# Performance work log

Measured on AMD Instinct MI355X. Metric: run time of the kernel, lower is better.

Reference implementation:

```python
import jax, jax.numpy as jnp
import numpy as np

B, C, W, H = 4, 256, 64, 64
N = W * H
SCALE = 0.02  # keep QK^T energies in a stable softmax range


def setup_inputs() -> dict:
    key = jax.random.key(0)
    ks = jax.random.split(key, 8)
    return {
        "x": jax.random.normal(ks[0], (B, C, W, H), jnp.float32),
        "geo_embed": jax.random.normal(ks[1], (B, N, C), jnp.float32),
        "Wq": jax.random.normal(ks[2], (C, C), jnp.float32) * SCALE,
        "bq": jnp.zeros((C,), jnp.float32),
        "Wk": jax.random.normal(ks[3], (C, C), jnp.float32) * SCALE,
        "bk": jnp.zeros((C,), jnp.float32),
        "Wv": jax.random.normal(ks[4], (C, C), jnp.float32) * SCALE,
        "bv": jnp.zeros((C,), jnp.float32),
        "Wgp": jax.random.normal(ks[5], (C, C), jnp.float32) * SCALE,
        "bgp": jnp.zeros((C,), jnp.float32),
        "Wgg": jax.random.normal(ks[6], (1, 2 * C), jnp.float32) * SCALE,
        "bgg": jnp.zeros((1,), jnp.float32),
    }


def reference(x, geo_embed, Wq, bq, Wk, bk, Wv, bv, Wgp, bgp, Wgg, bgg):
    b, c, w, h = x.shape
    n = w * h
    xf = x.reshape(b, c, n)  # [B, C, N]

    # 1x1 conv == per-pixel linear; q laid out [B, N, O] (permuted in torch)
    q = jnp.einsum("oc,bcn->bno", Wq, xf) + bq  # [B, N, O]

    # geo gating on the query
    ge = geo_embed @ Wgp.T + bgp  # [B, N, O]
    gate = jax.nn.sigmoid(jnp.concatenate([q, ge], axis=-1) @ Wgg.T + bgg)  # [B, N, 1]
    q = q + gate * ge

    k = jnp.einsum("oc,bcn->bon", Wk, xf) + bk[:, None]  # [B, O, N]
    v = jnp.einsum("oc,bcn->bon", Wv, xf) + bv[:, None]  # [B, C, N]

    energy = jnp.einsum("bno,bom->bnm", q, k)  # [B, N, N]
    attention = jax.nn.softmax(energy, axis=-1)

    # out = bmm(value, attention^T): out[b,c,m] = sum_n v[b,c,n] * attention[b,m,n]
    out = jnp.einsum("bcn,bmn->bcm", v, attention).reshape(b, c, w, h)

    # output gating: torch .view reinterpretation of (B, N, O) as (B, C, W, H)
    ge_r = ge.reshape(b, c, w, h)
    out = out * (1.0 + jax.nn.sigmoid(ge_r))
    return out, attention
```

## Files before the change

### kernel.cpp

```cpp
#include <hip/hip_runtime.h>
#include <hip/hip_bf16.h>
#include <math.h>

static constexpr int BB = 4;
static constexpr int CC = 256;
static constexpr int NN = 4096;

using bf16   = __bf16;
using f16    = _Float16;
using bf16x8 = __attribute__((ext_vector_type(8))) __bf16;
using bf16x4 = __attribute__((ext_vector_type(4))) __bf16;
using f16x8  = __attribute__((ext_vector_type(8))) _Float16;
using f16x4  = __attribute__((ext_vector_type(4))) _Float16;
using f32x4  = __attribute__((ext_vector_type(4))) float;

__device__ inline void gload_lds16(const void* g, void* l) {
  __builtin_amdgcn_global_load_lds(
      (const __attribute__((address_space(1))) void*)g,
      (__attribute__((address_space(3))) void*)l, 16, 0, 0);
}

__device__ inline void swz_bid(int& xb, int& yb, int& zb) {
  int gx = gridDim.x, gy = gridDim.y;
  int nwg = gx * gy * (int)gridDim.z;
  int flat = blockIdx.x + gx * (blockIdx.y + gy * blockIdx.z);
  int q = nwg >> 3;
  int w = (flat & 7) * q + (flat >> 3);
  xb = w % gx;
  int r = w / gx;
  yb = r % gy;
  zb = r / gy;
}

__global__ __launch_bounds__(256) void cvt_weights_kernel(
    const float* __restrict__ w0, const float* __restrict__ w1,
    const float* __restrict__ w2, const float* __restrict__ w3,
    bf16* __restrict__ out) {
  const float* srcs[4] = {w0, w1, w2, w3};
  const float* s = srcs[blockIdx.y];
  bf16* dst = out + (size_t)blockIdx.y * (CC * CC);
  int i = (blockIdx.x * 256 + threadIdx.x) * 4;
  float4 v = *(const float4*)(s + i);
  bf16x4 t;
  t[0] = (bf16)v.x; t[1] = (bf16)v.y; t[2] = (bf16)v.z; t[3] = (bf16)v.w;
  *(bf16x4*)(dst + i) = t;
}

__global__ __launch_bounds__(256) void cvt_f32_bf16_kernel(
    const float* __restrict__ in, bf16* __restrict__ out, long n) {
  long i = ((long)blockIdx.x * blockDim.x + threadIdx.x) * 4;
  if (i >= n) return;
  float4 v = *(const float4*)(in + i);
  bf16x4 t;
  t[0] = (bf16)v.x; t[1] = (bf16)v.y; t[2] = (bf16)v.z; t[3] = (bf16)v.w;
  *(bf16x4*)(out + i) = t;
}

__global__ __launch_bounds__(256) void transpose_x_kernel(
    const float* __restrict__ x, bf16* __restrict__ xt) {
  __shared__ float tile[64][65];
  int b  = blockIdx.z;
  int c0 = blockIdx.x * 64;
  int n0 = blockIdx.y * 64;
  const float* xp = x  + (long)b * CC * NN;
  bf16*       xtp = xt + (long)b * NN * CC;
  int tj = threadIdx.x & 63;
  int ti = threadIdx.x >> 6;
#pragma unroll
  for (int p = 0; p < 16; ++p) {
    int i = ti + p * 4;
    tile[i][tj] = xp[(long)(c0 + i) * NN + n0 + tj];
  }
  __syncthreads();
#pragma unroll
  for (int p = 0; p < 16; ++p) {
    int i = ti + p * 4;
    xtp[(long)(n0 + i) * CC + c0 + tj] = (bf16)tile[tj][i];
  }
}

__global__ __launch_bounds__(256) void proj_all_kernel(
    const bf16* __restrict__ xt, const bf16* __restrict__ geob,
    const bf16* __restrict__ Wall,
    const float* __restrict__ bq, const float* __restrict__ bgp,
    const float* __restrict__ bk, const float* __restrict__ bv,
    bf16* __restrict__ qn, float* __restrict__ ge,
    bf16* __restrict__ kn, bf16* __restrict__ vb) {
  __shared__ bf16 As[128 * 32];
  __shared__ bf16 Bs[128 * 32];
  const long NCst = (long)NN * CC;
  const int bz = blockIdx.z;
  const int b = bz >> 2, p = bz & 3;
  const bf16 *Ap, *Bp;
  const float* bias;
  int row0, col0;
  if (p == 3) {
    Ap = Wall + 2 * CC * CC;
    Bp = xt + b * NCst;
    bias = bv;
    row0 = blockIdx.x * 128;
    col0 = blockIdx.y * 128;
  } else {
    Ap = (p == 1 ? geob : xt) + b * NCst;
    Bp = Wall + (size_t)(p == 0 ? 0 : (p == 1 ? 3 : 1)) * CC * CC;
    bias = (p == 0 ? bq : (p == 1 ? bgp : bk));
    row0 = blockIdx.y * 128;
    col0 = blockIdx.x * 128;
  }

  const int t   = threadIdx.x;
  const int wid = t >> 6;
  const int l   = t & 63;
  const int lr  = l & 15;
  const int lk  = (l >> 4) * 8;
  const int warow = (wid >> 1) * 64;
  const int wbcol = (wid & 1) * 64;
  const int srow = t >> 2;
  const int scol = (t & 3) * 8;

  f32x4 acc[4][4];
#pragma unroll
  for (int i = 0; i < 4; ++i)
#pragma unroll
    for (int j = 0; j < 4; ++j) acc[i][j] = {0.f, 0.f, 0.f, 0.f};

  for (int k0 = 0; k0 < CC; k0 += 32) {
    __syncthreads();
#pragma unroll
    for (int q = 0; q < 2; ++q)
      gload_lds16(Ap + (long)(row0 + srow + 64 * q) * CC + k0 + scol,
                  As + ((q * 256 + t) * 8));
#pragma unroll
    for (int q = 0; q < 2; ++q)
      gload_lds16(Bp + (long)(col0 + srow + 64 * q) * CC + k0 + scol,
                  Bs + ((q * 256 + t) * 8));
    __syncthreads();
    bf16x8 a[4], bb[4];
#pragma unroll
    for (int i = 0; i < 4; ++i)
      a[i] = *(const bf16x8*)(As + (warow + 16 * i + lr) * 32 + lk);
#pragma unroll
    for (int j = 0; j < 4; ++j)
      bb[j] = *(const bf16x8*)(Bs + (wbcol + 16 * j + lr) * 32 + lk);
#pragma unroll
    for (int i = 0; i < 4; ++i)
#pragma unroll
      for (int j = 0; j < 4; ++j)
        acc[i][j] = __builtin_amdgcn_mfma_f32_16x16x32_bf16(a[i], bb[j], acc[i][j], 0, 0, 0);
  }

  const int orow = (l >> 4) * 4;
  const int ocol = l & 15;
#pragma unroll
  for (int i = 0; i < 4; ++i) {
#pragma unroll
    for (int j = 0; j < 4; ++j) {
      int colb = col0 + wbcol + 16 * j + ocol;
#pragma unroll
      for (int r = 0; r < 4; ++r) {
        int row = row0 + warow + 16 * i + orow + r;
        if (p == 3) {
          float vv = acc[i][j][r] + bias[row];
          vb[b * NCst + (long)row * NN + colb] = (bf16)vv;
        } else {
          float vv = acc[i][j][r] + bias[colb];
          long di = b * NCst + (long)row * CC + colb;
          if (p == 1)
            ge[di] = vv;
          else
            (p == 0 ? qn : kn)[di] = (bf16)vv;
        }
      }
    }
  }
}

template <int BIAS_MODE, int B_MODE, int OUT_MODE, bool GATE_EPI, bool SWZ, bool STAT>
__global__ __launch_bounds__(256) void gemm_nt_lds(
    const bf16* __restrict__ A, const void* __restrict__ Bm,
    const float* __restrict__ bias, void* __restrict__ D,
    const float* __restrict__ gefl, float2* __restrict__ pstat,
    int Ncols, int K, long sA, long sB, long sD, long sGe) {
  __shared__ bf16 As[128 * 32];
  __shared__ bf16 Bs[128 * 32];
  int bx = blockIdx.x, by = blockIdx.y, bz = blockIdx.z;
  if constexpr (SWZ) swz_bid(bx, by, bz);
  const bf16* Ab = A + (long)bz * sA;
  const float* geb = GATE_EPI ? (gefl + bz * sGe) : nullptr;

  const int t   = threadIdx.x;
  const int wid = t >> 6;
  const int l   = t & 63;
  const int lr  = l & 15;
  const int lk  = (l >> 4) * 8;
  const int row0 = by * 128;
  const int col0 = bx * 128;
  const int warow = (wid >> 1) * 64;
  const int wbcol = (wid & 1) * 64;

  const int srow = t >> 2;
  const int scol = (t & 3) * 8;
  const int frow = t >> 3;
  const int fc4  = (t & 7) * 4;

  f32x4 acc[4][4];
#pragma unroll
  for (int i = 0; i < 4; ++i)
#pragma unroll
    for (int j = 0; j < 4; ++j) acc[i][j] = {0.f, 0.f, 0.f, 0.f};

  for (int k0 = 0; k0 < K; k0 += 32) {
    __syncthreads();
#pragma unroll
    for (int p = 0; p < 2; ++p)
      gload_lds16(Ab + (long)(row0 + srow + 64 * p) * K + k0 + scol,
                  As + ((p * 256 + t) * 8));
    if constexpr (B_MODE == 0) {
      const bf16* Bb = (const bf16*)Bm + (long)bz * sB;
#pragma unroll
      for (int p = 0; p < 2; ++p)
        gload_lds16(Bb + (long)(col0 + srow + 64 * p) * K + k0 + scol,
                    Bs + ((p * 256 + t) * 8));
    } else {
      const float* Bf = (const float*)Bm + (long)bz * sB;
#pragma unroll
      for (int p = 0; p < 4; ++p) {
        float4 u = *(const float4*)(Bf + (long)(col0 + frow + 32 * p) * K + k0 + fc4);
        bf16x4 tv;
        tv[0] = (bf16)u.x; tv[1] = (bf16)u.y; tv[2] = (bf16)u.z; tv[3] = (bf16)u.w;
        *(bf16x4*)(Bs + (frow + 32 * p) * 32 + fc4) = tv;
      }
    }
    __syncthreads();
    bf16x8 a[4], bb[4];
#pragma unroll
    for (int i = 0; i < 4; ++i)
      a[i] = *(const bf16x8*)(As + (warow + 16 * i + lr) * 32 + lk);
#pragma unroll
    for (int j = 0; j < 4; ++j)
      bb[j] = *(const bf16x8*)(Bs + (wbcol + 16 * j + lr) * 32 + lk);
#pragma unroll
    for (int i = 0; i < 4; ++i)
#pragma unroll
      for (int j = 0; j < 4; ++j)
        acc[i][j] = __builtin_amdgcn_mfma_f32_16x16x32_bf16(a[i], bb[j], acc[i][j], 0, 0, 0);
  }

  const int orow = (l >> 4) * 4;
  const int ocol = l & 15;
#pragma unroll
  for (int i = 0; i < 4; ++i) {
#pragma unroll
    for (int j = 0; j < 4; ++j) {
      int colb = col0 + wbcol + 16 * j + ocol;
#pragma unroll
      for (int r = 0; r < 4; ++r) {
        int row = row0 + warow + 16 * i + orow + r;
        float vv = acc[i][j][r];
        if constexpr (BIAS_MODE == 1) vv += bias[colb];
        if constexpr (BIAS_MODE == 2) vv += bias[row];
        if constexpr (GATE_EPI) {
          float g = geb[(long)row * 4096 + colb];
          vv *= 1.f + 1.f / (1.f + __expf(-g));
        }
        long di = bz * sD + (long)row * Ncols + colb;
        if constexpr (OUT_MODE == 0)
          ((float*)D)[di] = vv;
        else if constexpr (OUT_MODE == 1)
          ((bf16*)D)[di] = (bf16)vv;
        else
          ((f16*)D)[di] = (f16)vv;
      }
    }
  }

  if constexpr (STAT) {
    __shared__ float2 sm[128][2];
#pragma unroll
    for (int i = 0; i < 4; ++i) {
#pragma unroll
      for (int r = 0; r < 4; ++r) {
        float m = fmaxf(fmaxf(acc[i][0][r], acc[i][1][r]),
                        fmaxf(acc[i][2][r], acc[i][3][r]));
#pragma unroll
        for (int s = 8; s >= 1; s >>= 1) m = fmaxf(m, __shfl_xor(m, s, 64));
        float sum = 0.f;
#pragma unroll
        for (int j = 0; j < 4; ++j) sum += __expf(acc[i][j][r] - m);
#pragma unroll
        for (int s = 8; s >= 1; s >>= 1) sum += __shfl_xor(sum, s, 64);
        if ((l & 15) == 0) {
          int Rl = warow + 16 * i + (l >> 4) * 4 + r;
          sm[Rl][wid & 1] = make_float2(m, sum);
        }
      }
    }
    __syncthreads();
    if (t < 128) {
      float2 a2 = sm[t][0], b2 = sm[t][1];
      float m = fmaxf(a2.x, b2.x);
      float s = a2.y * __expf(a2.x - m) + b2.y * __expf(b2.x - m);
      pstat[((long)bz * NN + row0 + t) * 32 + bx] = make_float2(m, s);
    }
  }
}

__global__ __launch_bounds__(256) void rowstat_reduce_kernel(
    const float2* __restrict__ pstat, float2* __restrict__ minv) {
  int row = blockIdx.x * 4 + (threadIdx.x >> 6);
  int l = threadIdx.x & 63;
  float2 v = (l < 32) ? pstat[(long)row * 32 + l] : make_float2(-1e30f, 0.f);
  float m = v.x;
#pragma unroll
  for (int s = 16; s >= 1; s >>= 1) m = fmaxf(m, __shfl_xor(m, s, 64));
  float sum = v.y * __expf(v.x - m);
#pragma unroll
  for (int s = 16; s >= 1; s >>= 1) sum += __shfl_xor(sum, s, 64);
  if (l == 0) minv[row] = make_float2(m, 1.f / sum);
}

template <bool SWZ>
__global__ __launch_bounds__(512) void pv_fused_kernel(
    const bf16* __restrict__ V, const f16* __restrict__ E,
    const float2* __restrict__ minv, float* __restrict__ attn,
    float* __restrict__ pbuf) {
  __shared__ bf16 Bs[2][64 * 64];
  int bx = blockIdx.x, by = blockIdx.y, bz = blockIdx.z;
  if constexpr (SWZ) swz_bid(bx, by, bz);
  const int mrow0 = bx * 64;
  const int KBASE = by * (NN / 2);
  const long NCst = (long)NN * CC;
  const long NNst = (long)NN * NN;
  const bf16* Vb = V + bz * NCst;
  const f16*  Eb = E + bz * NNst;
  float* attnb = attn + bz * NNst;
  float* pb = pbuf + (long)(bz * 2 + by) * NCst;

  const int t   = threadIdx.x;
  const int wid = t >> 6;
  const int l   = t & 63;
  const int lr  = l & 15;
  const int lk8 = l >> 4;
  const int crow = wid * 32;

  const int rE = t >> 3;
  const int q4 = (t & 7) * 4;
  const float2 mi = minv[(long)bz * NN + mrow0 + rE];
  const f16* Erow = Eb + (long)(mrow0 + rE) * NN + q4;
  float* Arow = attnb + (long)(mrow0 + rE) * NN + q4;
  const int c8a = (t & 7) >> 1;
  const int o4  = (t & 1) * 4;
  const int woff1 = rE * 64 + ((c8a ^ (rE & 7)) << 3) + o4;
  const int woff2 = rE * 64 + (((c8a + 4) ^ (rE & 7)) << 3) + o4;

  const bf16* Vr0 = Vb + (long)(crow + lr) * NN + lk8 * 8;
  const bf16* Vr1 = Vb + (long)(crow + 16 + lr) * NN + lk8 * 8;

  f32x4 acc[2][4];
#pragma unroll
  for (int i = 0; i < 2; ++i)
#pragma unroll
    for (int j = 0; j < 4; ++j) acc[i][j] = {0.f, 0.f, 0.f, 0.f};

  f16x4 elo = *(const f16x4*)(Erow + KBASE);
  f16x4 ehi = *(const f16x4*)(Erow + KBASE + 32);

  auto produce = [&](int kdst, int buf) {
    float pl[4], ph[4];
#pragma unroll
    for (int i = 0; i < 4; ++i) pl[i] = __expf((float)elo[i] - mi.x) * mi.y;
#pragma unroll
    for (int i = 0; i < 4; ++i) ph[i] = __expf((float)ehi[i] - mi.x) * mi.y;
    float4 u0 = {pl[0], pl[1], pl[2], pl[3]};
    float4 u1 = {ph[0], ph[1], ph[2], ph[3]};
    *(float4*)(Arow + kdst)      = u0;
    *(float4*)(Arow + kdst + 32) = u1;
    bf16x4 b0, b1;
#pragma unroll
    for (int i = 0; i < 4; ++i) { b0[i] = (bf16)pl[i]; b1[i] = (bf16)ph[i]; }
    *(bf16x4*)(&Bs[buf][woff1]) = b0;
    *(bf16x4*)(&Bs[buf][woff2]) = b1;
    int kn = (kdst + 64) & (NN - 1);
    elo = *(const f16x4*)(Erow + kn);
    ehi = *(const f16x4*)(Erow + kn + 32);
  };

  auto consume = [&](int buf, bf16x8 a00, bf16x8 a01, bf16x8 a10, bf16x8 a11) {
    const bf16* B0 = &Bs[buf][0];
#pragma unroll
    for (int j = 0; j < 4; ++j) {
      int Rb = 16 * j + lr;
      bf16x8 b0 = *(const bf16x8*)(B0 + Rb * 64 + ((lk8 ^ (Rb & 7)) * 8));
      bf16x8 b1 = *(const bf16x8*)(B0 + Rb * 64 + (((lk8 + 4) ^ (Rb & 7)) * 8));
      acc[0][j] = __builtin_amdgcn_mfma_f32_16x16x32_bf16(a00, b0, acc[0][j], 0, 0, 0);
      acc[1][j] = __builtin_amdgcn_mfma_f32_16x16x32_bf16(a10, b0, acc[1][j], 0, 0, 0);
      acc[0][j] = __builtin_amdgcn_mfma_f32_16x16x32_bf16(a01, b1, acc[0][j], 0, 0, 0);
      acc[1][j] = __builtin_amdgcn_mfma_f32_16x16x32_bf16(a11, b1, acc[1][j], 0, 0, 0);
    }
  };

#define LOADV(k0, A0, A1, A2, A3)                  \
  A0 = *(const bf16x8*)(Vr0 + (k0));               \
  A1 = *(const bf16x8*)(Vr0 + (k0) + 32);          \
  A2 = *(const bf16x8*)(Vr1 + (k0));               \
  A3 = *(const bf16x8*)(Vr1 + (k0) + 32);

#define FENCE_BAR()                                         \
  asm volatile("s_waitcnt lgkmcnt(0)" ::: "memory");        \
  __builtin_amdgcn_s_barrier();                             \
  __builtin_amdgcn_sched_barrier(0);

  bf16x8 A00, A01, A10, A11, B00, B01, B10, B11;

  produce(KBASE, 0);
  LOADV(KBASE, A00, A01, A10, A11);
  FENCE_BAR();

  for (int it = 0; it < 15; ++it) {
    int k0 = KBASE + it * 128;
    LOADV(k0 + 64, B00, B01, B10, B11);
    consume(0, A00, A01, A10, A11);
    produce(k0 + 64, 1);
    FENCE_BAR();
    LOADV(k0 + 128, A00, A01, A10, A11);
    consume(1, B00, B01, B10, B11);
    produce(k0 + 128, 0);
    FENCE_BAR();
  }
  LOADV(KBASE + 1984, B00, B01, B10, B11);
  consume(0, A00, A01, A10, A11);
  produce(KBASE + 1984, 1);
  FENCE_BAR();
  consume(1, B00, B01, B10, B11);
#undef LOADV
#undef FENCE_BAR

  const int orow = (l >> 4) * 4;
  const int ocol = l & 15;
#pragma unroll
  for (int i = 0; i < 2; ++i) {
#pragma unroll
    for (int j = 0; j < 4; ++j) {
      int m = mrow0 + 16 * j + ocol;
#pragma unroll
      for (int r = 0; r < 4; ++r) {
        int c = crow + 16 * i + orow + r;
        pb[(long)c * 4096 + m] = acc[i][j][r];
      }
    }
  }
}

__global__ __launch_bounds__(256) void combine_kernel(
    const float* __restrict__ pbuf, const float* __restrict__ ge,
    float* __restrict__ out) {
  const long NCst = (long)NN * CC;
  long i = ((long)blockIdx.x * 256 + threadIdx.x) * 8;
  int b = (int)(i >> 20);
  long r = i & (NCst - 1);
  const float* p0 = pbuf + (long)(b * 2) * NCst + r;
  const float* p1 = p0 + NCst;
  const float* g  = ge + (long)b * NCst + r;
  float* o = out + i;
#pragma unroll
  for (int h = 0; h < 2; ++h) {
    float4 a = *(const float4*)(p0 + h * 4);
    float4 c = *(const float4*)(p1 + h * 4);
    float4 gv = *(const float4*)(g + h * 4);
    float4 u;
    u.x = (a.x + c.x) * (1.f + 1.f / (1.f + __expf(-gv.x)));
    u.y = (a.y + c.y) * (1.f + 1.f / (1.f + __expf(-gv.y)));
    u.z = (a.z + c.z) * (1.f + 1.f / (1.f + __expf(-gv.z)));
    u.w = (a.w + c.w) * (1.f + 1.f / (1.f + __expf(-gv.w)));
    *(float4*)(o + h * 4) = u;
  }
}

__global__ __launch_bounds__(256) void gate_kernel(
    bf16* __restrict__ q, const float* __restrict__ ge,
    const float* __restrict__ Wgg, const float* __restrict__ bgg) {
  int row = blockIdx.x * 4 + (threadIdx.x >> 6);
  int l = threadIdx.x & 63;
  bf16* qr = q + (long)row * 256;
  const float* ger = ge + (long)row * 256;
  float s = 0.f;
  float qv[4], gv[4];
#pragma unroll
  for (int i = 0; i < 4; ++i) {
    int o = l + 64 * i;
    qv[i] = (float)qr[o];
    gv[i] = ger[o];
    s += qv[i] * Wgg[o] + gv[i] * Wgg[256 + o];
  }
#pragma unroll
  for (int m = 32; m >= 1; m >>= 1) s += __shfl_xor(s, m, 64);
  float gate = 1.f / (1.f + __expf(-(s + bgg[0])));
#pragma unroll
  for (int i = 0; i < 4; ++i) {
    int o = l + 64 * i;
    qr[o] = (bf16)(qv[i] + gate * gv[i]);
  }
}

__global__ __launch_bounds__(256) void softmax32_kernel(float* __restrict__ attn) {
  long row = blockIdx.x;
  float* p = attn + row * 4096;
  int t = threadIdx.x;
  __shared__ float red[8];
  float4 v[4];
  float mx = -1e30f;
#pragma unroll
  for (int c = 0; c < 4; ++c) {
    v[c] = *(const float4*)(p + c * 1024 + t * 4);
    mx = fmaxf(mx, fmaxf(fmaxf(v[c].x, v[c].y), fmaxf(v[c].z, v[c].w)));
  }
#pragma unroll
  for (int m = 32; m >= 1; m >>= 1) mx = fmaxf(mx, __shfl_xor(mx, m, 64));
  if ((t & 63) == 0) red[t >> 6] = mx;
  __syncthreads();
  mx = fmaxf(fmaxf(red[0], red[1]), fmaxf(red[2], red[3]));
  float sum = 0.f;
#pragma unroll
  for (int c = 0; c < 4; ++c) {
    v[c].x = __expf(v[c].x - mx);
    v[c].y = __expf(v[c].y - mx);
    v[c].z = __expf(v[c].z - mx);
    v[c].w = __expf(v[c].w - mx);
    sum += v[c].x + v[c].y + v[c].z + v[c].w;
  }
#pragma unroll
  for (int m = 32; m >= 1; m >>= 1) sum += __shfl_xor(sum, m, 64);
  if ((t & 63) == 0) red[4 + (t >> 6)] = sum;
  __syncthreads();
  float inv = 1.f / (red[4] + red[5] + red[6] + red[7]);
#pragma unroll
  for (int c = 0; c < 4; ++c) {
    v[c].x *= inv; v[c].y *= inv; v[c].z *= inv; v[c].w *= inv;
    *(float4*)(p + c * 1024 + t * 4) = v[c];
  }
}

extern "C" void kernel_launch(void* const* d_in, const int* in_sizes, int n_in,
                              void* d_out, int out_size, void* d_ws, size_t ws_size,
                              hipStream_t stream) {
  const float* x    = (const float*)d_in[0];
  const float* geo  = (const float*)d_in[1];
  const float* Wq   = (const float*)d_in[2];
  const float* bq   = (const float*)d_in[3];
  const float* Wk   = (const float*)d_in[4];
  const float* bk   = (const float*)d_in[5];
  const float* Wv   = (const float*)d_in[6];
  const float* bv   = (const float*)d_in[7];
  const float* Wgp  = (const float*)d_in[8];
  const float* bgp  = (const float*)d_in[9];
  const float* Wgg  = (const float*)d_in[10];
  const float* bgg  = (const float*)d_in[11];

  float* out  = (float*)d_out;
  float* attn = out + (long)BB * CC * NN;

  char* w = (char*)d_ws;
  size_t used = 0;
  auto alloc = [&](size_t bytes) {
    char* p = w + used;
    used += (bytes + 255) & ~(size_t)255;
    return p;
  };
  bf16*  xt   = (bf16*)alloc((size_t)BB * NN * CC * 2);
  bf16*  geob = (bf16*)alloc((size_t)BB * NN * CC * 2);
  bf16*  qn   = (bf16*)alloc((size_t)BB * NN * CC * 2);
  bf16*  kn   = (bf16*)alloc((size_t)BB * NN * CC * 2);
  bf16*  vb   = (bf16*)alloc((size_t)BB * CC * NN * 2);
  float* ge   = (float*)alloc((size_t)BB * NN * CC * 4);
  bf16*  Wall = (bf16*)alloc((size_t)4 * CC * CC * 2);
  bf16*  Wvb  = Wall + 2 * CC * CC;
  size_t abf_bytes   = (size_t)BB * NN * NN * 2;
  size_t pstat_bytes = (size_t)BB * NN * 32 * sizeof(float2);
  size_t minv_bytes  = (size_t)BB * NN * sizeof(float2);
  size_t pbuf_bytes  = (size_t)BB * 2 * NN * CC * 4;
  bool big = (ws_size >=
              used + abf_bytes + pstat_bytes + minv_bytes + pbuf_bytes + 2048);
  f16* abf = nullptr;
  float2* pstat = nullptr;
  float2* minv = nullptr;
  float* pbuf = nullptr;
  if (big) {
    abf   = (f16*)alloc(abf_bytes);
    pstat = (float2*)alloc(pstat_bytes);
    minv  = (float2*)alloc(minv_bytes);
    pbuf  = (float*)alloc(pbuf_bytes);
  }

  const long NCst = (long)NN * CC;
  const long NNst = (long)NN * NN;

  cvt_weights_kernel<<<dim3(64, 4), 256, 0, stream>>>(Wq, Wk, Wv, Wgp, Wall);
  cvt_f32_bf16_kernel<<<(BB * NCst) / 1024, 256, 0, stream>>>(geo, geob, BB * NCst);
  transpose_x_kernel<<<dim3(4, 64, BB), 256, 0, stream>>>(x, xt);

  proj_all_kernel<<<dim3(2, 32, BB * 4), 256, 0, stream>>>(
      xt, geob, Wall, bq, bgp, bk, bv, qn, ge, kn, vb);
  gate_kernel<<<(BB * NN) / 4, 256, 0, stream>>>(qn, ge, Wgg, bgg);

  if (big) {
    gemm_nt_lds<0, 0, 2, false, true, true><<<dim3(32, 32, BB), 256, 0, stream>>>(
        qn, kn, nullptr, abf, nullptr, pstat, NN, CC, NCst, NCst, NNst, 0);
    rowstat_reduce_kernel<<<(BB * NN) / 4, 256, 0, stream>>>(pstat, minv);
    pv_fused_kernel<true><<<dim3(64, 2, BB), 512, 0, stream>>>(
        vb, abf, minv, attn, pbuf);
    combine_kernel<<<(int)((long)BB * NCst / (256 * 8)), 256, 0, stream>>>(
        pbuf, ge, out);
  } else {
    gemm_nt_lds<0, 0, 0, false, true, false><<<dim3(32, 32, BB), 256, 0, stream>>>(
        qn, kn, nullptr, attn, nullptr, nullptr, NN, CC, NCst, NCst, NNst, 0);
    softmax32_kernel<<<BB * NN, 256, 0, stream>>>(attn);
    gemm_nt_lds<0, 1, 0, true, true, false><<<dim3(32, 2, BB), 256, 0, stream>>>(
        vb, attn, nullptr, out, ge, nullptr, NN, NN, NCst, NNst, NCst, NCst);
  }
}
```

Before: 300.3 us.

## Fuse geo bf16 conversion into projection and halve PV fused tile rows

Drops the separate fp32-to-bf16 kernel for geo_embed. The projection kernel now loads fp32 geo rows directly, converts them in registers and stores bf16 into LDS, which removes one launch and a round trip through global memory. It also halves the M tile of the fused softmax-PV kernel from 64 to 32 rows and doubles its grid, giving more workgroups. The trade-off is that each V tile loaded from global memory is reused over fewer rows, so V is read more times in total.

```diff
diff --git a/kernel.cpp b/kernel.cpp
--- a/kernel.cpp
+++ b/kernel.cpp
@@ -46,16 +46,6 @@
   *(bf16x4*)(dst + i) = t;
 }
 
-__global__ __launch_bounds__(256) void cvt_f32_bf16_kernel(
-    const float* __restrict__ in, bf16* __restrict__ out, long n) {
-  long i = ((long)blockIdx.x * blockDim.x + threadIdx.x) * 4;
-  if (i >= n) return;
-  float4 v = *(const float4*)(in + i);
-  bf16x4 t;
-  t[0] = (bf16)v.x; t[1] = (bf16)v.y; t[2] = (bf16)v.z; t[3] = (bf16)v.w;
-  *(bf16x4*)(out + i) = t;
-}
-
 __global__ __launch_bounds__(256) void transpose_x_kernel(
     const float* __restrict__ x, bf16* __restrict__ xt) {
   __shared__ float tile[64][65];
@@ -80,7 +70,7 @@
 }
 
 __global__ __launch_bounds__(256) void proj_all_kernel(
-    const bf16* __restrict__ xt, const bf16* __restrict__ geob,
+    const bf16* __restrict__ xt, const float* __restrict__ geo,
     const bf16* __restrict__ Wall,
     const float* __restrict__ bq, const float* __restrict__ bgp,
     const float* __restrict__ bk, const float* __restrict__ bv,
@@ -91,7 +81,8 @@
   const long NCst = (long)NN * CC;
   const int bz = blockIdx.z;
   const int b = bz >> 2, p = bz & 3;
-  const bf16 *Ap, *Bp;
+  const bf16 *Ap = nullptr, *Bp;
+  const float* Af32 = nullptr;
   const float* bias;
   int row0, col0;
   if (p == 3) {
@@ -101,7 +92,8 @@
     row0 = blockIdx.x * 128;
     col0 = blockIdx.y * 128;
   } else {
-    Ap = (p == 1 ? geob : xt) + b * NCst;
+    if (p == 1) Af32 = geo + b * NCst;
+    else        Ap   = xt + b * NCst;
     Bp = Wall + (size_t)(p == 0 ? 0 : (p == 1 ? 3 : 1)) * CC * CC;
     bias = (p == 0 ? bq : (p == 1 ? bgp : bk));
     row0 = blockIdx.y * 128;
@@ -117,6 +109,8 @@
   const int wbcol = (wid & 1) * 64;
   const int srow = t >> 2;
   const int scol = (t & 3) * 8;
+  const int frow = t >> 3;
+  const int fc4  = (t & 7) * 4;
 
   f32x4 acc[4][4];
 #pragma unroll
@@ -126,10 +120,20 @@
 
   for (int k0 = 0; k0 < CC; k0 += 32) {
     __syncthreads();
-#pragma unroll
-    for (int q = 0; q < 2; ++q)
-      gload_lds16(Ap + (long)(row0 + srow + 64 * q) * CC + k0 + scol,
-                  As + ((q * 256 + t) * 8));
+    if (p == 1) {
+#pragma unroll
+      for (int q = 0; q < 4; ++q) {
+        float4 u = *(const float4*)(Af32 + (long)(row0 + frow + 32 * q) * CC + k0 + fc4);
+        bf16x4 tv;
+        tv[0] = (bf16)u.x; tv[1] = (bf16)u.y; tv[2] = (bf16)u.z; tv[3] = (bf16)u.w;
+        *(bf16x4*)(As + (frow + 32 * q) * 32 + fc4) = tv;
+      }
+    } else {
+#pragma unroll
+      for (int q = 0; q < 2; ++q)
+        gload_lds16(Ap + (long)(row0 + srow + 64 * q) * CC + k0 + scol,
+                    As + ((q * 256 + t) * 8));
+    }
 #pragma unroll
     for (int q = 0; q < 2; ++q)
       gload_lds16(Bp + (long)(col0 + srow + 64 * q) * CC + k0 + scol,
@@ -324,10 +328,10 @@
     const bf16* __restrict__ V, const f16* __restrict__ E,
     const float2* __restrict__ minv, float* __restrict__ attn,
     float* __restrict__ pbuf) {
-  __shared__ bf16 Bs[2][64 * 64];
+  __shared__ bf16 Bs[2][32 * 64];
   int bx = blockIdx.x, by = blockIdx.y, bz = blockIdx.z;
   if constexpr (SWZ) swz_bid(bx, by, bz);
-  const int mrow0 = bx * 64;
+  const int mrow0 = bx * 32;
   const int KBASE = by * (NN / 2);
   const long NCst = (long)NN * CC;
   const long NNst = (long)NN * NN;
@@ -343,52 +347,44 @@
   const int lk8 = l >> 4;
   const int crow = wid * 32;
 
-  const int rE = t >> 3;
-  const int q4 = (t & 7) * 4;
+  const int rE = t >> 4;
+  const int q4 = (t & 15) * 4;
   const float2 mi = minv[(long)bz * NN + mrow0 + rE];
   const f16* Erow = Eb + (long)(mrow0 + rE) * NN + q4;
   float* Arow = attnb + (long)(mrow0 + rE) * NN + q4;
-  const int c8a = (t & 7) >> 1;
+  const int c8a = (t & 15) >> 1;
   const int o4  = (t & 1) * 4;
-  const int woff1 = rE * 64 + ((c8a ^ (rE & 7)) << 3) + o4;
-  const int woff2 = rE * 64 + (((c8a + 4) ^ (rE & 7)) << 3) + o4;
+  const int woff = rE * 64 + ((c8a ^ (rE & 7)) << 3) + o4;
 
   const bf16* Vr0 = Vb + (long)(crow + lr) * NN + lk8 * 8;
   const bf16* Vr1 = Vb + (long)(crow + 16 + lr) * NN + lk8 * 8;
 
-  f32x4 acc[2][4];
+  f32x4 acc[2][2];
 #pragma unroll
   for (int i = 0; i < 2; ++i)
 #pragma unroll
-    for (int j = 0; j < 4; ++j) acc[i][j] = {0.f, 0.f, 0.f, 0.f};
-
-  f16x4 elo = *(const f16x4*)(Erow + KBASE);
-  f16x4 ehi = *(const f16x4*)(Erow + KBASE + 32);
+    for (int j = 0; j < 2; ++j) acc[i][j] = {0.f, 0.f, 0.f, 0.f};
+
+  f16x4 ecur = *(const f16x4*)(Erow + KBASE);
 
   auto produce = [&](int kdst, int buf) {
-    float pl[4], ph[4];
-#pragma unroll
-    for (int i = 0; i < 4; ++i) pl[i] = __expf((float)elo[i] - mi.x) * mi.y;
-#pragma unroll
-    for (int i = 0; i < 4; ++i) ph[i] = __expf((float)ehi[i] - mi.x) * mi.y;
-    float4 u0 = {pl[0], pl[1], pl[2], pl[3]};
-    float4 u1 = {ph[0], ph[1], ph[2], ph[3]};
-    *(float4*)(Arow + kdst)      = u0;
-    *(float4*)(Arow + kdst + 32) = u1;
-    bf16x4 b0, b1;
-#pragma unroll
-    for (int i = 0; i < 4; ++i) { b0[i] = (bf16)pl[i]; b1[i] = (bf16)ph[i]; }
-    *(bf16x4*)(&Bs[buf][woff1]) = b0;
-    *(bf16x4*)(&Bs[buf][woff2]) = b1;
+    float pv[4];
+#pragma unroll
+    for (int i = 0; i < 4; ++i) pv[i] = __expf((float)ecur[i] - mi.x) * mi.y;
+    float4 u0 = {pv[0], pv[1], pv[2], pv[3]};
+    *(float4*)(Arow + kdst) = u0;
+    bf16x4 b0;
+#pragma unroll
+    for (int i = 0; i < 4; ++i) b0[i] = (bf16)pv[i];
+    *(bf16x4*)(&Bs[buf][woff]) = b0;
     int kn = (kdst + 64) & (NN - 1);
-    elo = *(const f16x4*)(Erow + kn);
-    ehi = *(const f16x4*)(Erow + kn + 32);
+    ecur = *(const f16x4*)(Erow + kn);
   };
 
   auto consume = [&](int buf, bf16x8 a00, bf16x8 a01, bf16x8 a10, bf16x8 a11) {
     const bf16* B0 = &Bs[buf][0];
 #pragma unroll
-    for (int j = 0; j < 4; ++j) {
+    for (int j = 0; j < 2; ++j) {
       int Rb = 16 * j + lr;
       bf16x8 b0 = *(const bf16x8*)(B0 + Rb * 64 + ((lk8 ^ (Rb & 7)) * 8));
       bf16x8 b1 = *(const bf16x8*)(B0 + Rb * 64 + (((lk8 + 4) ^ (Rb & 7)) * 8));
@@ -440,7 +436,7 @@
 #pragma unroll
   for (int i = 0; i < 2; ++i) {
 #pragma unroll
-    for (int j = 0; j < 4; ++j) {
+    for (int j = 0; j < 2; ++j) {
       int m = mrow0 + 16 * j + ocol;
 #pragma unroll
       for (int r = 0; r < 4; ++r) {
@@ -567,13 +563,11 @@
     return p;
   };
   bf16*  xt   = (bf16*)alloc((size_t)BB * NN * CC * 2);
-  bf16*  geob = (bf16*)alloc((size_t)BB * NN * CC * 2);
   bf16*  qn   = (bf16*)alloc((size_t)BB * NN * CC * 2);
   bf16*  kn   = (bf16*)alloc((size_t)BB * NN * CC * 2);
   bf16*  vb   = (bf16*)alloc((size_t)BB * CC * NN * 2);
   float* ge   = (float*)alloc((size_t)BB * NN * CC * 4);
   bf16*  Wall = (bf16*)alloc((size_t)4 * CC * CC * 2);
-  bf16*  Wvb  = Wall + 2 * CC * CC;
   size_t abf_bytes   = (size_t)BB * NN * NN * 2;
   size_t pstat_bytes = (size_t)BB * NN * 32 * sizeof(float2);
   size_t minv_bytes  = (size_t)BB * NN * sizeof(float2);
@@ -595,18 +589,17 @@
   const long NNst = (long)NN * NN;
 
   cvt_weights_kernel<<<dim3(64, 4), 256, 0, stream>>>(Wq, Wk, Wv, Wgp, Wall);
-  cvt_f32_bf16_kernel<<<(BB * NCst) / 1024, 256, 0, stream>>>(geo, geob, BB * NCst);
   transpose_x_kernel<<<dim3(4, 64, BB), 256, 0, stream>>>(x, xt);
 
   proj_all_kernel<<<dim3(2, 32, BB * 4), 256, 0, stream>>>(
-      xt, geob, Wall, bq, bgp, bk, bv, qn, ge, kn, vb);
+      xt, geo, Wall, bq, bgp, bk, bv, qn, ge, kn, vb);
   gate_kernel<<<(BB * NN) / 4, 256, 0, stream>>>(qn, ge, Wgg, bgg);
 
   if (big) {
     gemm_nt_lds<0, 0, 2, false, true, true><<<dim3(32, 32, BB), 256, 0, stream>>>(
         qn, kn, nullptr, abf, nullptr, pstat, NN, CC, NCst, NCst, NNst, 0);
     rowstat_reduce_kernel<<<(BB * NN) / 4, 256, 0, stream>>>(pstat, minv);
-    pv_fused_kernel<true><<<dim3(64, 2, BB), 512, 0, stream>>>(
+    pv_fused_kernel<true><<<dim3(128, 2, BB), 512, 0, stream>>>(
         vb, abf, minv, attn, pbuf);
     combine_kernel<<<(int)((long)BB * NCst / (256 * 8)), 256, 0, stream>>>(
         pbuf, ge, out);
```

New measurement: 344.4 us. 14.7% more time.
